# Kernel optimization log

Measured on AMD Instinct MI355X. Metric: run time of the kernel, lower is better.

The kernel has to match this reference:

```python
import jax, jax.numpy as jnp
import numpy as np

GROUPS = 256   # B: number of index groups
SEQ = 512      # L: tokens per group (equal-length groups)
D_IN = 128
D_QK = 64
D_V = 128


def setup_inputs() -> dict:
    key = jax.random.key(0)
    ks = jax.random.split(key, 7)
    N = GROUPS * SEQ
    inputs = jax.random.normal(ks[0], (N, D_IN), dtype=jnp.float32)
    # sorted group ids: GROUPS groups of SEQ tokens each
    index = jnp.repeat(jnp.arange(GROUPS, dtype=jnp.int64), SEQ)
    s_in = 1.0 / np.sqrt(D_IN)
    Wq = jax.random.normal(ks[1], (D_IN, D_QK), dtype=jnp.float32) * s_in
    bq = jax.random.normal(ks[2], (D_QK,), dtype=jnp.float32) * 0.01
    Wk = jax.random.normal(ks[3], (D_IN, D_QK), dtype=jnp.float32) * s_in
    bk = jax.random.normal(ks[4], (D_QK,), dtype=jnp.float32) * 0.01
    Wv = jax.random.normal(ks[5], (D_IN, D_V), dtype=jnp.float32) * s_in
    bv = jax.random.normal(ks[6], (D_V,), dtype=jnp.float32) * 0.01
    return {"inputs": inputs, "index": index, "Wq": Wq, "bq": bq,
            "Wk": Wk, "bk": bk, "Wv": Wv, "bv": bv}


def reference(inputs, index, Wq, bq, Wk, bk, Wv, bv):
    # Linear projections on flat tokens [N, d]
    q = inputs @ Wq + bq          # [N, D_QK]
    k = inputs @ Wk + bk          # [N, D_QK]
    v = inputs @ Wv + bv          # [N, D_V]
    # unbatch: equal-length sorted groups -> [B, L, d]
    q = q.reshape(GROUPS, SEQ, D_QK)
    k = k.reshape(GROUPS, SEQ, D_QK)
    v = v.reshape(GROUPS, SEQ, D_V)
    # note the module's scale: sqrt(2 * d_qk)
    scale = 1.0 / np.sqrt(2.0 * D_QK).astype(np.float32)
    scores = jnp.einsum('bqd,bkd->bqk', q, k) * scale   # [B, L, L]
    attn = jax.nn.softmax(scores, axis=-1)
    out = jnp.einsum('bqk,bkd->bqd', attn, v)           # [B, L, D_V]
    return out.reshape(-1, D_V)                          # [N, D_V]
```

## Files before the change

kernel.cpp:

```cpp
#include <hip/hip_runtime.h>
#include <hip/hip_bf16.h>
#include <stdint.h>

#define GROUPS 256
#define SEQ    512
#define D_IN   128
#define D_QK   64
#define D_V    128
#define NTOK   (GROUPS * SEQ)

typedef short bf8 __attribute__((ext_vector_type(8)));
typedef short bf4 __attribute__((ext_vector_type(4)));
typedef float f32x4 __attribute__((ext_vector_type(4)));

__device__ __forceinline__ short f2bf(float f) {
    __bf16 h = (__bf16)f;
    return __builtin_bit_cast(short, h);
}

__device__ __forceinline__ void gload_lds16(const void* g, void* l) {
    __builtin_amdgcn_global_load_lds(
        (const __attribute__((address_space(1))) unsigned int*)(uintptr_t)(g),
        (__attribute__((address_space(3))) unsigned int*)(uint32_t)(uintptr_t)(l),
        16, 0, 0);
}

__global__ __launch_bounds__(256) void prep_w(
    const float* __restrict__ Wq, const float* __restrict__ bq,
    const float* __restrict__ Wk, const float* __restrict__ bk,
    const float* __restrict__ Wv, const float* __restrict__ bv,
    short* __restrict__ Wt, float* __restrict__ bcat)
{
    const int t = blockIdx.x * 256 + threadIdx.x;
    const int r  = t >> 5;
    const int k0 = (t & 31) * 4;
    const float* W; int ld; int c;
    if (r < 64)       { W = Wq; ld = 64;  c = r; }
    else if (r < 128) { W = Wk; ld = 64;  c = r - 64; }
    else              { W = Wv; ld = 128; c = r - 128; }
    bf4 pk;
#pragma unroll
    for (int i = 0; i < 4; ++i) pk[i] = f2bf(W[(size_t)(k0 + i) * ld + c]);
    const int phys = (k0 * 2) ^ ((r & 7) << 4);
    *reinterpret_cast<bf4*>((char*)Wt + r * 256 + phys) = pk;
    if (t < 256) {
        const float* b = (t < 64) ? bq : (t < 128 ? bk : bv);
        const int cb   = (t < 64) ? t  : (t < 128 ? t - 64 : t - 128);
        bcat[t] = b[cb];
    }
}

__global__ __launch_bounds__(256) void proj_kernel(
    const float* __restrict__ x, const short* __restrict__ Wt,
    const float* __restrict__ bcat,
    short* __restrict__ Q, short* __restrict__ K, short* __restrict__ Vt)
{
    __shared__ short wlds[32768];
    const int tid = threadIdx.x;
    const int wid = tid >> 6, lane = tid & 63, l15 = lane & 15, lg = lane >> 4;

#pragma unroll
    for (int i = 0; i < 16; ++i)
        gload_lds16((const char*)Wt + i * 4096 + tid * 16,
                    (char*)wlds + i * 4096 + tid * 16);

    const size_t tw = (size_t)blockIdx.x * 256 + wid * 64;
    const int g     = (int)(tw >> 9);
    const int tseg  = (int)(tw & 511);

    bf8 xf[4][4];
#pragma unroll
    for (int m = 0; m < 4; ++m) {
        const float* xr = x + (tw + m * 16 + l15) * D_IN;
#pragma unroll
        for (int kf = 0; kf < 4; ++kf) {
            const float4 a = *reinterpret_cast<const float4*>(xr + kf * 32 + lg * 8);
            const float4 b = *reinterpret_cast<const float4*>(xr + kf * 32 + lg * 8 + 4);
            bf8 v;
            v[0] = f2bf(a.x); v[1] = f2bf(a.y); v[2] = f2bf(a.z); v[3] = f2bf(a.w);
            v[4] = f2bf(b.x); v[5] = f2bf(b.y); v[6] = f2bf(b.z); v[7] = f2bf(b.w);
            xf[m][kf] = v;
        }
    }
    __syncthreads();

#pragma unroll
    for (int cf = 0; cf < 16; ++cf) {
        const int wrow = cf * 16 + l15;
        bf8 wf[4];
#pragma unroll
        for (int kf = 0; kf < 4; ++kf) {
            const int off = (kf * 64 + lg * 16) ^ ((wrow & 7) << 4);
            wf[kf] = *reinterpret_cast<const bf8*>((const char*)wlds + wrow * 256 + off);
        }

        if (cf < 8) {
            const float4 bias4 = *reinterpret_cast<const float4*>(bcat + cf * 16 + lg * 4);
#pragma unroll
            for (int m = 0; m < 4; ++m) {
                f32x4 acc = (f32x4){0.f, 0.f, 0.f, 0.f};
#pragma unroll
                for (int kf = 0; kf < 4; ++kf)
                    acc = __builtin_amdgcn_mfma_f32_16x16x32_bf16(wf[kf], xf[m][kf], acc, 0, 0, 0);
                bf4 pk;
                pk[0] = f2bf(acc[0] + bias4.x); pk[1] = f2bf(acc[1] + bias4.y);
                pk[2] = f2bf(acc[2] + bias4.z); pk[3] = f2bf(acc[3] + bias4.w);
                const size_t tok = tw + m * 16 + l15;
                if (cf < 4) {
                    *reinterpret_cast<bf4*>((char*)Q + tok * 128 + cf * 32 + lg * 8) = pk;
                } else {
                    const int lo = ((cf - 4) * 32 + lg * 8) ^ (((int)tok & 7) << 4);
                    *reinterpret_cast<bf4*>((char*)K + tok * 128 + lo) = pk;
                }
            }
        } else {
            const int d = (cf - 8) * 16 + l15;
            const float bias = bcat[cf * 16 + l15];
            char* vrow = (char*)Vt + (((size_t)g * D_V + d) << 10);
#pragma unroll
            for (int m = 0; m < 4; ++m) {
                f32x4 acc = (f32x4){0.f, 0.f, 0.f, 0.f};
#pragma unroll
                for (int kf = 0; kf < 4; ++kf)
                    acc = __builtin_amdgcn_mfma_f32_16x16x32_bf16(xf[m][kf], wf[kf], acc, 0, 0, 0);
                bf4 pk;
#pragma unroll
                for (int r = 0; r < 4; ++r) pk[r] = f2bf(acc[r] + bias);
                const int t0    = tseg + m * 16;
                const int blk32 = t0 >> 5;
                const int half  = (t0 >> 4) & 1;
                const int logi  = blk32 * 64 + lg * 16 + half * 8;
                const int phys  = (logi & ~127) | ((logi & 127) ^ ((d & 7) << 4));
                *reinterpret_cast<bf4*>(vrow + phys) = pk;
            }
        }
    }
}

__global__ __launch_bounds__(512) void attn_kernel(
    const short* __restrict__ Q, const short* __restrict__ K,
    const short* __restrict__ Vt, float* __restrict__ out)
{
    __shared__ short lds[2 * 12288];
    const int g = blockIdx.x, rb = blockIdx.y;
    const int tid = threadIdx.x, wid = tid >> 6, lane = tid & 63;
    const int l15 = lane & 15, lg = lane >> 4;
    const size_t gtok = (size_t)g * SEQ;
    const int row0 = rb * 256 + wid * 32;

    bf8 qf[2][2];
#pragma unroll
    for (int rf = 0; rf < 2; ++rf) {
        const short* qr = Q + (gtok + row0 + rf * 16 + l15) * 64 + lg * 8;
        qf[rf][0] = *reinterpret_cast<const bf8*>(qr);
        qf[rf][1] = *reinterpret_cast<const bf8*>(qr + 32);
    }

    const char* Kg = (const char*)(K + gtok * 64);
    const char* Vg = (const char*)(Vt + ((size_t)g * D_V << 9));

    f32x4 o[2][8];
#pragma unroll
    for (int rf = 0; rf < 2; ++rf)
#pragma unroll
        for (int vt = 0; vt < 8; ++vt) o[rf][vt] = (f32x4){0.f, 0.f, 0.f, 0.f};
    float psum[2] = {0.f, 0.f};
    const float sl2e = 0.08838834764831845f * 1.4426950408889634f;

    auto stage = [&](int kt, int b) {
        char* lbase = (char*)lds + b * 24576;
        int c = wid * 3;
#pragma unroll
        for (int i = 0; i < 3; ++i, ++c) {
            if (c < 8) {
                gload_lds16(Kg + (size_t)kt * 8192 + c * 1024 + lane * 16,
                            lbase + c * 1024 + lane * 16);
            } else {
                const int cv = c - 8;
                const int d  = cv * 8 + (lane >> 3);
                gload_lds16(Vg + (size_t)d * 1024 + kt * 128 + (lane & 7) * 16,
                            lbase + 8192 + cv * 1024 + lane * 16);
            }
        }
    };

    auto compute = [&](int b) {
        const char* lb = (const char*)lds + b * 24576;
        f32x4 st[4][2];
#pragma unroll
        for (int tf = 0; tf < 4; ++tf) {
            const int tok = tf * 16 + l15;
            const char* kb = lb + tok * 128;
            const int x7 = (tok & 7) << 4;
            const bf8 k0 = *reinterpret_cast<const bf8*>(kb + ((lg * 16) ^ x7));
            const bf8 k1 = *reinterpret_cast<const bf8*>(kb + ((64 + lg * 16) ^ x7));
#pragma unroll
            for (int rf = 0; rf < 2; ++rf) {
                f32x4 s = (f32x4){0.f, 0.f, 0.f, 0.f};
                s = __builtin_amdgcn_mfma_f32_16x16x32_bf16(k0, qf[rf][0], s, 0, 0, 0);
                s = __builtin_amdgcn_mfma_f32_16x16x32_bf16(k1, qf[rf][1], s, 0, 0, 0);
                st[tf][rf] = s;
            }
        }
        bf8 pa[2][2];
#pragma unroll
        for (int rf = 0; rf < 2; ++rf) {
#pragma unroll
            for (int ks = 0; ks < 2; ++ks) {
                bf8 pv;
#pragma unroll
                for (int i = 0; i < 4; ++i) {
                    const float p0 = __builtin_amdgcn_exp2f(st[2 * ks][rf][i] * sl2e);
                    const float p1 = __builtin_amdgcn_exp2f(st[2 * ks + 1][rf][i] * sl2e);
                    psum[rf] += p0 + p1;
                    pv[i] = f2bf(p0); pv[i + 4] = f2bf(p1);
                }
                pa[rf][ks] = pv;
            }
        }
        const char* vb = lb + 8192;
#pragma unroll
        for (int vt = 0; vt < 8; ++vt) {
            const int d = vt * 16 + l15;
            const char* vr = vb + d * 128;
            const int x7 = (d & 7) << 4;
            const bf8 v0 = *reinterpret_cast<const bf8*>(vr + ((lg * 16) ^ x7));
            const bf8 v1 = *reinterpret_cast<const bf8*>(vr + ((64 + lg * 16) ^ x7));
            o[0][vt] = __builtin_amdgcn_mfma_f32_16x16x32_bf16(pa[0][0], v0, o[0][vt], 0, 0, 0);
            o[1][vt] = __builtin_amdgcn_mfma_f32_16x16x32_bf16(pa[1][0], v0, o[1][vt], 0, 0, 0);
            o[0][vt] = __builtin_amdgcn_mfma_f32_16x16x32_bf16(pa[0][1], v1, o[0][vt], 0, 0, 0);
            o[1][vt] = __builtin_amdgcn_mfma_f32_16x16x32_bf16(pa[1][1], v1, o[1][vt], 0, 0, 0);
        }
    };

    stage(0, 0);
    stage(1, 1);
#pragma unroll 1
    for (int kt = 0; kt < 8; ++kt) {
        const int b = kt & 1;
        if (kt < 7) { asm volatile("s_waitcnt vmcnt(3)" ::: "memory"); }
        else        { asm volatile("s_waitcnt vmcnt(0)" ::: "memory"); }
        __builtin_amdgcn_s_barrier();
        compute(b);
        if (kt + 2 < 8) {
            asm volatile("" ::: "memory");
            __builtin_amdgcn_s_barrier();
            stage(kt + 2, b);
        }
    }

#pragma unroll
    for (int rf = 0; rf < 2; ++rf) {
        psum[rf] += __shfl_xor(psum[rf], 16);
        psum[rf] += __shfl_xor(psum[rf], 32);
    }
#pragma unroll
    for (int rf = 0; rf < 2; ++rf) {
        float linv[4];
#pragma unroll
        for (int r = 0; r < 4; ++r) linv[r] = 1.0f / __shfl(psum[rf], lg * 4 + r);
        float* op = out + (gtok + row0 + rf * 16) * D_V;
#pragma unroll
        for (int vt = 0; vt < 8; ++vt)
#pragma unroll
            for (int r = 0; r < 4; ++r)
                op[(size_t)(lg * 4 + r) * D_V + vt * 16 + l15] = o[rf][vt][r] * linv[r];
    }
}

extern "C" void kernel_launch(void* const* d_in, const int* in_sizes, int n_in,
                              void* d_out, int out_size, void* d_ws, size_t ws_size,
                              hipStream_t stream) {
    (void)in_sizes; (void)n_in; (void)ws_size; (void)out_size;
    const float* x  = (const float*)d_in[0];
    const float* Wq = (const float*)d_in[2];
    const float* bq = (const float*)d_in[3];
    const float* Wk = (const float*)d_in[4];
    const float* bk = (const float*)d_in[5];
    const float* Wv = (const float*)d_in[6];
    const float* bv = (const float*)d_in[7];
    float* out = (float*)d_out;

    short* Qw = (short*)d_ws;
    short* Kw = Qw + (size_t)NTOK * D_QK;
    short* Vt = Kw + (size_t)NTOK * D_QK;

    short* Wt   = (short*)out;
    float* bcat = (float*)((char*)out + 65536);

    prep_w<<<32, 256, 0, stream>>>(Wq, bq, Wk, bk, Wv, bv, Wt, bcat);
    proj_kernel<<<NTOK / 256, 256, 0, stream>>>(x, Wt, bcat, Qw, Kw, Vt);
    attn_kernel<<<dim3(GROUPS, 2), 512, 0, stream>>>(Qw, Kw, Vt, out);
}
```

Baseline: 75.72 us.

## Fold softmax scale into Q weights, MFMA row sums, smaller attention blocks

Folds the softmax scale and log2(e) into the Q projection weights and bias so the attention loop applies exp2 directly to the scores without a multiply. Row sums of the probabilities are now computed with an extra MFMA against a ones vector, which replaces the scalar accumulation and the cross-lane shuffles. Attention blocks shrink from 512 to 256 threads with four row-blocks per group and a launch-bounds occupancy hint, and each wave stages twice as many loads. The trade-off is more K/V tile reloads across blocks and some extra MFMA work, in exchange for fewer VALU ops and potentially higher occupancy.

```diff
diff --git a/kernel.cpp b/kernel.cpp
--- a/kernel.cpp
+++ b/kernel.cpp
@@ -8,6 +8,8 @@
 #define D_QK   64
 #define D_V    128
 #define NTOK   (GROUPS * SEQ)
+
+#define SL2E (0.08838834764831845f * 1.4426950408889634f)
 
 typedef short bf8 __attribute__((ext_vector_type(8)));
 typedef short bf4 __attribute__((ext_vector_type(4)));
@@ -34,19 +36,19 @@
     const int t = blockIdx.x * 256 + threadIdx.x;
     const int r  = t >> 5;
     const int k0 = (t & 31) * 4;
-    const float* W; int ld; int c;
-    if (r < 64)       { W = Wq; ld = 64;  c = r; }
-    else if (r < 128) { W = Wk; ld = 64;  c = r - 64; }
-    else              { W = Wv; ld = 128; c = r - 128; }
+    const float* W; int ld; int c; float sc;
+    if (r < 64)       { W = Wq; ld = 64;  c = r;       sc = SL2E; }
+    else if (r < 128) { W = Wk; ld = 64;  c = r - 64;  sc = 1.0f; }
+    else              { W = Wv; ld = 128; c = r - 128; sc = 1.0f; }
     bf4 pk;
 #pragma unroll
-    for (int i = 0; i < 4; ++i) pk[i] = f2bf(W[(size_t)(k0 + i) * ld + c]);
+    for (int i = 0; i < 4; ++i) pk[i] = f2bf(W[(size_t)(k0 + i) * ld + c] * sc);
     const int phys = (k0 * 2) ^ ((r & 7) << 4);
     *reinterpret_cast<bf4*>((char*)Wt + r * 256 + phys) = pk;
     if (t < 256) {
         const float* b = (t < 64) ? bq : (t < 128 ? bk : bv);
         const int cb   = (t < 64) ? t  : (t < 128 ? t - 64 : t - 128);
-        bcat[t] = b[cb];
+        bcat[t] = b[cb] * (t < 64 ? SL2E : 1.0f);
     }
 }
 
@@ -137,7 +139,7 @@
     }
 }
 
-__global__ __launch_bounds__(512) void attn_kernel(
+__global__ __launch_bounds__(256, 3) void attn_kernel(
     const short* __restrict__ Q, const short* __restrict__ K,
     const short* __restrict__ Vt, float* __restrict__ out)
 {
@@ -146,7 +148,7 @@
     const int tid = threadIdx.x, wid = tid >> 6, lane = tid & 63;
     const int l15 = lane & 15, lg = lane >> 4;
     const size_t gtok = (size_t)g * SEQ;
-    const int row0 = rb * 256 + wid * 32;
+    const int row0 = rb * 128 + wid * 32;
 
     bf8 qf[2][2];
 #pragma unroll
@@ -164,14 +166,14 @@
     for (int rf = 0; rf < 2; ++rf)
 #pragma unroll
         for (int vt = 0; vt < 8; ++vt) o[rf][vt] = (f32x4){0.f, 0.f, 0.f, 0.f};
-    float psum[2] = {0.f, 0.f};
-    const float sl2e = 0.08838834764831845f * 1.4426950408889634f;
+    f32x4 psv[2] = {(f32x4){0.f, 0.f, 0.f, 0.f}, (f32x4){0.f, 0.f, 0.f, 0.f}};
+    const bf8 onesf = {0x3F80, 0x3F80, 0x3F80, 0x3F80, 0x3F80, 0x3F80, 0x3F80, 0x3F80};
 
     auto stage = [&](int kt, int b) {
         char* lbase = (char*)lds + b * 24576;
-        int c = wid * 3;
-#pragma unroll
-        for (int i = 0; i < 3; ++i, ++c) {
+        int c = wid * 6;
+#pragma unroll
+        for (int i = 0; i < 6; ++i, ++c) {
             if (c < 8) {
                 gload_lds16(Kg + (size_t)kt * 8192 + c * 1024 + lane * 16,
                             lbase + c * 1024 + lane * 16);
@@ -210,12 +212,11 @@
                 bf8 pv;
 #pragma unroll
                 for (int i = 0; i < 4; ++i) {
-                    const float p0 = __builtin_amdgcn_exp2f(st[2 * ks][rf][i] * sl2e);
-                    const float p1 = __builtin_amdgcn_exp2f(st[2 * ks + 1][rf][i] * sl2e);
-                    psum[rf] += p0 + p1;
-                    pv[i] = f2bf(p0); pv[i + 4] = f2bf(p1);
+                    pv[i]     = f2bf(__builtin_amdgcn_exp2f(st[2 * ks][rf][i]));
+                    pv[i + 4] = f2bf(__builtin_amdgcn_exp2f(st[2 * ks + 1][rf][i]));
                 }
                 pa[rf][ks] = pv;
+                psv[rf] = __builtin_amdgcn_mfma_f32_16x16x32_bf16(pv, onesf, psv[rf], 0, 0, 0);
             }
         }
         const char* vb = lb + 8192;
@@ -238,9 +239,10 @@
 #pragma unroll 1
     for (int kt = 0; kt < 8; ++kt) {
         const int b = kt & 1;
-        if (kt < 7) { asm volatile("s_waitcnt vmcnt(3)" ::: "memory"); }
+        if (kt < 7) { asm volatile("s_waitcnt vmcnt(6)" ::: "memory"); }
         else        { asm volatile("s_waitcnt vmcnt(0)" ::: "memory"); }
         __builtin_amdgcn_s_barrier();
+        asm volatile("" ::: "memory");
         compute(b);
         if (kt + 2 < 8) {
             asm volatile("" ::: "memory");
@@ -251,14 +253,9 @@
 
 #pragma unroll
     for (int rf = 0; rf < 2; ++rf) {
-        psum[rf] += __shfl_xor(psum[rf], 16);
-        psum[rf] += __shfl_xor(psum[rf], 32);
-    }
-#pragma unroll
-    for (int rf = 0; rf < 2; ++rf) {
         float linv[4];
 #pragma unroll
-        for (int r = 0; r < 4; ++r) linv[r] = 1.0f / __shfl(psum[rf], lg * 4 + r);
+        for (int r = 0; r < 4; ++r) linv[r] = 1.0f / psv[rf][r];
         float* op = out + (gtok + row0 + rf * 16) * D_V;
 #pragma unroll
         for (int vt = 0; vt < 8; ++vt)
@@ -290,5 +287,5 @@
 
     prep_w<<<32, 256, 0, stream>>>(Wq, bq, Wk, bk, Wv, bv, Wt, bcat);
     proj_kernel<<<NTOK / 256, 256, 0, stream>>>(x, Wt, bcat, Qw, Kw, Vt);
-    attn_kernel<<<dim3(GROUPS, 2), 512, 0, stream>>>(Qw, Kw, Vt, out);
-}
+    attn_kernel<<<dim3(GROUPS, 4), 256, 0, stream>>>(Qw, Kw, Vt, out);
+}
```

Result: no change. 75.81 us (+0.1%).
